# Performance work log

Hardware: AMD Instinct MI355X
Metric: run time of the kernel (lower is better)

## Reference

```python
import jax, jax.numpy as jnp
import numpy as np

ALPHA = 0.999
BETA = 8
GAMMA = 1
THRESHOLD = 0.5
BATCH, IN_DIM, N_RULES = 8192, 4096, 2048


def setup_inputs() -> dict:
    key = jax.random.key(0)
    kx, kw = jax.random.split(key)
    # x: fuzzy binary features in [0, 1]
    x = jax.random.uniform(kx, (BATCH, IN_DIM), dtype=jnp.float32)
    # W: learned weights, init uniform in [INIT_L=0, 0.5] as in the torch module
    W = 0.5 * jax.random.uniform(kw, (IN_DIM, N_RULES), dtype=jnp.float32)
    return {"x": x, "W": W}


def reference(x, W):
    # Module forward returns the binarized path's VALUE (GradGraft forwards X=res_bar).
    # binarized_forward: Wb = 1[W - 0.5 > 0]; res = (1 - x) @ Wb; out = 1[res <= 0]
    Wb = (W > THRESHOLD).astype(x.dtype)          # [IN_DIM, N_RULES]
    res = (1.0 - x) @ Wb                          # [BATCH, N_RULES]
    return jnp.where(res > 0, jnp.zeros((), x.dtype), jnp.ones((), x.dtype))
```

## Files before the change

### kernel.cpp

```cpp
#include <hip/hip_runtime.h>
#include <stdint.h>

#define BATCH   8192
#define IN_DIM  4096
#define N_RULES 2048
#define NW      (IN_DIM / 64)



__global__ __launch_bounds__(256) void pack_w_kernel(const float* __restrict__ W,
                                                     uint64_t* __restrict__ wt,
                                                     unsigned int* __restrict__ any_partial) {
    int t    = threadIdx.x;
    int lane = t & 63;
    int wid  = blockIdx.x * 4 + (t >> 6);
    int w     = wid >> 5;
    int jbase = (wid & 31) << 6;
    int j     = jbase + lane;

    const float* Wp = W + (size_t)(w * 64) * N_RULES + j;
    uint64_t word = 0;
#pragma unroll 8
    for (int k = 0; k < 64; ++k) {
        float v = Wp[(size_t)k * N_RULES];
        word |= (uint64_t)(v > 0.5f) << k;
    }
    wt[(size_t)w * N_RULES + j] = word;
    uint64_t nzmask = __ballot(word != 0);
    if (lane == 0) any_partial[wid] = (nzmask != 0) ? 1u : 0u;
}

#define BT 128
#define JT 64

__global__ __launch_bounds__(256) void conj_main(const float* __restrict__ x,
                                                 const uint64_t* __restrict__ wt,
                                                 const unsigned int* __restrict__ any_partial,
                                                 float* __restrict__ out) {
    __shared__ uint64_t wlds[JT][65];
    __shared__ uint64_t xw[BT];

    int t  = threadIdx.x;
    int bt = blockIdx.x & 63;
    int jt = blockIdx.x >> 6;
    int bbase = bt * BT;
    int jbase = jt * JT;

    float4* o4 = (float4*)out;
    const int ldo4 = N_RULES / 4;

    unsigned int av = any_partial[(t & 63) * 32 + jt];
    uint64_t nz = __ballot(av != 0);

    if (nz == 0) {
        float4 ones = make_float4(1.f, 1.f, 1.f, 1.f);
#pragma unroll
        for (int k = 0; k < 8; ++k) {
            int idx = k * 256 + t;
            int bl = idx >> 4, j4 = idx & 15;
            o4[(size_t)(bbase + bl) * ldo4 + (jbase >> 2) + j4] = ones;
        }
        return;
    }

#pragma unroll
    for (int k = 0; k < 16; ++k) {
        int idx = k * 256 + t;
        int jl = idx & 63, w = idx >> 6;
        wlds[jl][w] = wt[(size_t)w * N_RULES + jbase + jl];
    }

    int tj = (t & 15) * 4;
    int tb = (t >> 4) * 8;
    int wv   = t >> 6;
    int lane = t & 63;
    unsigned int acc = 0;

    for (int w = 0; w < 64; ++w) {
        __syncthreads();
        for (int r = wv; r < BT; r += 4) {
            uint64_t m = __ballot(x[(size_t)(bbase + r) * IN_DIM + w * 64 + lane] < 1.0f);
            if (lane == 0) xw[r] = m;
        }
        __syncthreads();

        uint64_t wj0 = wlds[tj + 0][w];
        uint64_t wj1 = wlds[tj + 1][w];
        uint64_t wj2 = wlds[tj + 2][w];
        uint64_t wj3 = wlds[tj + 3][w];
#pragma unroll
        for (int ib = 0; ib < 8; ++ib) {
            uint64_t xv = xw[tb + ib];
            unsigned int s = (unsigned)((xv & wj0) != 0)
                           | ((unsigned)((xv & wj1) != 0) << 1)
                           | ((unsigned)((xv & wj2) != 0) << 2)
                           | ((unsigned)((xv & wj3) != 0) << 3);
            acc |= s << (ib * 4);
        }
    }

#pragma unroll
    for (int ib = 0; ib < 8; ++ib) {
        float4 v;
        v.x = ((acc >> (ib * 4 + 0)) & 1) ? 0.f : 1.f;
        v.y = ((acc >> (ib * 4 + 1)) & 1) ? 0.f : 1.f;
        v.z = ((acc >> (ib * 4 + 2)) & 1) ? 0.f : 1.f;
        v.w = ((acc >> (ib * 4 + 3)) & 1) ? 0.f : 1.f;
        o4[(size_t)(bbase + tb + ib) * ldo4 + (jbase >> 2) + (t & 15)] = v;
    }
}

extern "C" void kernel_launch(void* const* d_in, const int* in_sizes, int n_in,
                              void* d_out, int out_size, void* d_ws, size_t ws_size,
                              hipStream_t stream) {
    const float* x = (const float*)d_in[0];
    const float* W = (const float*)d_in[1];
    float* out = (float*)d_out;

    unsigned char* ws  = (unsigned char*)d_ws;
    uint64_t*      wt  = (uint64_t*)ws;
    unsigned int*  anyp = (unsigned int*)(ws + (size_t)NW * N_RULES * sizeof(uint64_t));

    pack_w_kernel<<<512, 256, 0, stream>>>(W, wt, anyp);
    conj_main<<<64 * 32, 256, 0, stream>>>(x, wt, anyp, out);
}
```

Before: 202.0 us.

## Use a global any-nonzero flag for an all-ones fast path with row-block tiling

Each W-packing block now reduces its nonzero flags to a single per-block bit. The main kernel reduces those bits to one global flag, and when the binarized W is entirely zero it writes ones over a contiguous output slab. The general path is retiled so that each block handles four full batch rows across all rules, reading the packed W from global memory instead of a per-tile LDS copy. Since W is uniform in [0, 0.5], the fast path is expected to run almost always, so the kernel becomes essentially a memset of the output. The general path has much less reuse of W per block.

```diff
diff --git a/kernel.cpp b/kernel.cpp
--- a/kernel.cpp
+++ b/kernel.cpp
@@ -10,10 +10,12 @@
 
 __global__ __launch_bounds__(256) void pack_w_kernel(const float* __restrict__ W,
                                                      uint64_t* __restrict__ wt,
-                                                     unsigned int* __restrict__ any_partial) {
+                                                     unsigned int* __restrict__ anyb) {
+    __shared__ unsigned int s4[4];
     int t    = threadIdx.x;
     int lane = t & 63;
-    int wid  = blockIdx.x * 4 + (t >> 6);
+    int wv   = t >> 6;
+    int wid  = blockIdx.x * 4 + wv;
     int w     = wid >> 5;
     int jbase = (wid & 31) << 6;
     int j     = jbase + lane;
@@ -26,87 +28,60 @@
         word |= (uint64_t)(v > 0.5f) << k;
     }
     wt[(size_t)w * N_RULES + j] = word;
+
     uint64_t nzmask = __ballot(word != 0);
-    if (lane == 0) any_partial[wid] = (nzmask != 0) ? 1u : 0u;
+    if (lane == 0) s4[wv] = (nzmask != 0) ? 1u : 0u;
+    __syncthreads();
+    if (t == 0) anyb[blockIdx.x] = s4[0] | s4[1] | s4[2] | s4[3];
 }
 
-#define BT 128
-#define JT 64
+__global__ __launch_bounds__(256) void write_out(const float* __restrict__ x,
+                                                 const uint64_t* __restrict__ wt,
+                                                 const unsigned int* __restrict__ anyb,
+                                                 float* __restrict__ out) {
+    __shared__ unsigned int sW[4];
+    __shared__ uint64_t sxb[4][64];
 
-__global__ __launch_bounds__(256) void conj_main(const float* __restrict__ x,
-                                                 const uint64_t* __restrict__ wt,
-                                                 const unsigned int* __restrict__ any_partial,
-                                                 float* __restrict__ out) {
-    __shared__ uint64_t wlds[JT][65];
-    __shared__ uint64_t xw[BT];
+    int t    = threadIdx.x;
+    int lane = t & 63;
+    int wv   = t >> 6;
 
-    int t  = threadIdx.x;
-    int bt = blockIdx.x & 63;
-    int jt = blockIdx.x >> 6;
-    int bbase = bt * BT;
-    int jbase = jt * JT;
+    unsigned int a = anyb[t * 2] | anyb[t * 2 + 1];
+    uint64_t nz = __ballot(a != 0);
+    if (lane == 0) sW[wv] = (nz != 0) ? 1u : 0u;
+    __syncthreads();
+    unsigned int g = sW[0] | sW[1] | sW[2] | sW[3];
 
-    float4* o4 = (float4*)out;
-    const int ldo4 = N_RULES / 4;
-
-    unsigned int av = any_partial[(t & 63) * 32 + jt];
-    uint64_t nz = __ballot(av != 0);
-
-    if (nz == 0) {
+    if (g == 0) {
         float4 ones = make_float4(1.f, 1.f, 1.f, 1.f);
+        float4* o4 = (float4*)out + (size_t)blockIdx.x * 2048;
 #pragma unroll
-        for (int k = 0; k < 8; ++k) {
-            int idx = k * 256 + t;
-            int bl = idx >> 4, j4 = idx & 15;
-            o4[(size_t)(bbase + bl) * ldo4 + (jbase >> 2) + j4] = ones;
-        }
+        for (int k = 0; k < 8; ++k)
+            o4[k * 256 + t] = ones;
         return;
     }
 
-#pragma unroll
-    for (int k = 0; k < 16; ++k) {
-        int idx = k * 256 + t;
-        int jl = idx & 63, w = idx >> 6;
-        wlds[jl][w] = wt[(size_t)w * N_RULES + jbase + jl];
+    int b0 = blockIdx.x * 4;
+    for (int w = 0; w < 64; ++w) {
+        uint64_t m = __ballot(x[(size_t)(b0 + wv) * IN_DIM + w * 64 + lane] < 1.0f);
+        if (lane == 0) sxb[wv][w] = m;
     }
+    __syncthreads();
 
-    int tj = (t & 15) * 4;
-    int tb = (t >> 4) * 8;
-    int wv   = t >> 6;
-    int lane = t & 63;
-    unsigned int acc = 0;
-
-    for (int w = 0; w < 64; ++w) {
-        __syncthreads();
-        for (int r = wv; r < BT; r += 4) {
-            uint64_t m = __ballot(x[(size_t)(bbase + r) * IN_DIM + w * 64 + lane] < 1.0f);
-            if (lane == 0) xw[r] = m;
+    for (int k = 0; k < 8; ++k) {
+        int j = t + k * 256;
+        unsigned int r0 = 0, r1 = 0, r2 = 0, r3 = 0;
+        for (int w = 0; w < 64; ++w) {
+            uint64_t wj = wt[(size_t)w * N_RULES + j];
+            r0 |= (unsigned)((sxb[0][w] & wj) != 0);
+            r1 |= (unsigned)((sxb[1][w] & wj) != 0);
+            r2 |= (unsigned)((sxb[2][w] & wj) != 0);
+            r3 |= (unsigned)((sxb[3][w] & wj) != 0);
         }
-        __syncthreads();
-
-        uint64_t wj0 = wlds[tj + 0][w];
-        uint64_t wj1 = wlds[tj + 1][w];
-        uint64_t wj2 = wlds[tj + 2][w];
-        uint64_t wj3 = wlds[tj + 3][w];
-#pragma unroll
-        for (int ib = 0; ib < 8; ++ib) {
-            uint64_t xv = xw[tb + ib];
-            unsigned int s = (unsigned)((xv & wj0) != 0)
-                           | ((unsigned)((xv & wj1) != 0) << 1)
-                           | ((unsigned)((xv & wj2) != 0) << 2)
-                           | ((unsigned)((xv & wj3) != 0) << 3);
-            acc |= s << (ib * 4);
-        }
-    }
-
-#pragma unroll
-    for (int ib = 0; ib < 8; ++ib) {
-        float4 v;
-        v.x = ((acc >> (ib * 4 + 0)) & 1) ? 0.f : 1.f;
-        v.y = ((acc >> (ib * 4 + 1)) & 1) ? 0.f : 1.f;
-        v.z = ((acc >> (ib * 4 + 2)) & 1) ? 0.f : 1.f;
-        v.w = ((acc >> (ib * 4 + 3)) & 1) ? 0.f : 1.f;
-        o4[(size_t)(bbase + tb + ib) * ldo4 + (jbase >> 2) + (t & 15)] = v;
+        out[(size_t)(b0 + 0) * N_RULES + j] = r0 ? 0.f : 1.f;
+        out[(size_t)(b0 + 1) * N_RULES + j] = r1 ? 0.f : 1.f;
+        out[(size_t)(b0 + 2) * N_RULES + j] = r2 ? 0.f : 1.f;
+        out[(size_t)(b0 + 3) * N_RULES + j] = r3 ? 0.f : 1.f;
     }
 }
 
@@ -119,8 +94,8 @@
 
     unsigned char* ws  = (unsigned char*)d_ws;
     uint64_t*      wt  = (uint64_t*)ws;
-    unsigned int*  anyp = (unsigned int*)(ws + (size_t)NW * N_RULES * sizeof(uint64_t));
+    unsigned int*  anyb = (unsigned int*)(ws + (size_t)NW * N_RULES * sizeof(uint64_t));
 
-    pack_w_kernel<<<512, 256, 0, stream>>>(W, wt, anyp);
-    conj_main<<<64 * 32, 256, 0, stream>>>(x, wt, anyp, out);
+    pack_w_kernel<<<512, 256, 0, stream>>>(W, wt, anyb);
+    write_out<<<2048, 256, 0, stream>>>(x, wt, anyb, out);
 }
```

New measurement: 202.2 us. About the same (+0.1%).
